# Kernel tuning notes

Hardware: AMD Instinct MI355X
Metric: run time of the kernel (lower is better)

Reference implementation:

```python
import jax, jax.numpy as jnp
import numpy as np

V, E, H, D1, D2, C = 32000, 500, 500, 800, 100, 2
B, T = 64, 400


def setup_inputs() -> dict:
    key = jax.random.key(0)
    ks = jax.random.split(key, 12)
    s = lambda fan_in, fan_out: float(np.sqrt(6.0 / (fan_in + fan_out)))  # xavier uniform
    u = lambda k, shape, lim: jax.random.uniform(k, shape, jnp.float32, -lim, lim)
    X = jax.random.randint(ks[0], (B, T), 0, V, dtype=jnp.int32)
    embed = u(ks[1], (V, E), s(V, E))
    # TF LSTMCell: kernel [input+hidden, 4*hidden], bias zeros, gate order i,j,f,o
    k1 = u(ks[2], (E + H, 4 * H), s(E + H, 4 * H))
    b1 = jnp.zeros((4 * H,), jnp.float32)
    k2 = u(ks[3], (H + H, 4 * H), s(H + H, 4 * H))
    b2 = jnp.zeros((4 * H,), jnp.float32)
    w1 = u(ks[4], (H, D1), s(H, D1)); bw1 = jnp.zeros((D1,), jnp.float32)
    w2 = u(ks[5], (D1, D2), s(D1, D2)); bw2 = jnp.zeros((D2,), jnp.float32)
    wp = u(ks[6], (D2, C), s(D2, C)); bp = jnp.zeros((C,), jnp.float32)
    return dict(X=X, embed=embed, k1=k1, b1=b1, k2=k2, b2=b2,
                w1=w1, bw1=bw1, w2=w2, bw2=bw2, wp=wp, bp=bp)


def _lstm(x_tbe, kernel, bias, hsize):
    """x_tbe: [T,B,in]; TF LSTMCell math with forget_bias=1.0. Returns all h: [T,B,H]."""
    Bn = x_tbe.shape[1]
    c0 = jnp.zeros((Bn, hsize), x_tbe.dtype)
    h0 = jnp.zeros((Bn, hsize), x_tbe.dtype)

    def step(carry, x_t):
        c, h = carry
        z = jnp.concatenate([x_t, h], axis=-1) @ kernel + bias
        i, j, f, o = jnp.split(z, 4, axis=-1)
        c = jax.nn.sigmoid(f + 1.0) * c + jax.nn.sigmoid(i) * jnp.tanh(j)
        h = jax.nn.sigmoid(o) * jnp.tanh(c)
        return (c, h), h

    _, hs = jax.lax.scan(step, (c0, h0), x_tbe)
    return hs


def reference(X, embed, k1, b1, k2, b2, w1, bw1, w2, bw2, wp, bp):
    # inference mode: dropout is identity
    x = embed[X]                      # [B,T,E]
    x = jnp.transpose(x, (1, 0, 2))   # [T,B,E]
    hs1 = _lstm(x, k1, b1, H)         # [T,B,H]
    hs2 = _lstm(hs1, k2, b2, H)       # [T,B,H]
    last = hs2[-1]                    # [B,H] last-step output of layer 2
    d1 = jax.nn.relu(last @ w1 + bw1)
    d2 = jax.nn.relu(d1 @ w2 + bw2)
    logits = d2 @ wp + bp             # [B,C]
    return logits
```

## Files before the change

### kernel.cpp

```cpp
#include <hip/hip_runtime.h>


#define NTHR 512
#define Tn 400
#define Hn 500

#define OFF_H1 0
#define OFF_H2 256000
#define OFF_C1 512000
#define OFF_C2 768000
#define OFF_D1 1024000
#define OFF_D2 1228800
#define WS_ZERO 1024000

__device__ __forceinline__ float qreduce(float v) {
    int t = __builtin_amdgcn_update_dpp(0, __float_as_int(v), 0xB1, 0xF, 0xF, true);
    v += __int_as_float(t);
    t = __builtin_amdgcn_update_dpp(0, __float_as_int(v), 0x4E, 0xF, 0xF, true);
    v += __int_as_float(t);
    return v;
}

__device__ __forceinline__ int wrow_map(int r) {
    int r2 = (r >= 512) ? r - 12 : r;
    if ((r >= 500 && r < 512) || r >= 1012) r2 = 0;
    return r2;
}

extern "C" __global__ void __launch_bounds__(NTHR)
rnn_step(const int* __restrict__ X, const float* __restrict__ embed,
         const float* __restrict__ k1, const float* __restrict__ b1g,
         const float* __restrict__ k2, const float* __restrict__ b2g,
         char* __restrict__ ws, int s)
{
    __shared__ float s_x[16384];
    __shared__ float s_w[2][8192];

    float* h1b = (float*)(ws + OFF_H1);
    float* h2b = (float*)(ws + OFF_H2);

    const int bid = blockIdx.x;
    const int tid = threadIdx.x;
    const int rr_ = bid >> 3;
    const int slice = (bid & 7) * 8 + (rr_ >> 2);
    const int btile = rr_ & 3;
    const int L = slice >> 5;
    const int ut = slice & 31;
    const int b0 = btile * 16;

    const bool active = L ? (s >= 1) : (s < Tn);
    if (!active) return;

    const int w = tid >> 6;
    const int l = tid & 63;
    const int ks = l & 3;
    const int cg = (l >> 2) & 7;
    const int bg = l >> 5;

    const float* Wm = L ? k2 : k1;
    const float* bv = L ? b2g : b1g;
    double* cb = (double*)(ws + (L ? OFF_C2 : OFF_C1));

    const int cur = s & 1, prv = cur ^ 1;
    const float* h1p = h1b + prv * 32000;
    const float* h2p = h2b + prv * 32000;
    float* houtT = (L ? h2b : h1b) + cur * 32000;
    const int t = L ? (s - 1) : s;
    const float* hlow = h1p;
    const float* hhigh = L ? h2p : h1p;

    const int wdr = l >> 4;
    const int wcq = l & 15;
    const int c_l = (4 * wcq) ^ (wdr << 3);
    const int wcol = (c_l >> 4) * 500 + min(ut * 16 + (c_l & 15), 496);

    const int xdr = l >> 2;
    const int xq4 = (l & 3) * 4;

    if (w == 7) {
        if (L == 0) {
            const int eb = l & 15, r = 496 + (l >> 4);
            const float v = embed[(size_t)X[(b0 + eb) * Tn + t] * 500 + r];
            s_x[r * 16 + eb] = v;
        } else {
            if (l < 16) {
                const int r = 496 + (l >> 2);
                const float4 v = *(const float4*)(hlow + r * 64 + b0 + (l & 3) * 4);
                *(float4*)&s_x[r * 16 + (l & 3) * 4] = v;
            }
        }
        if (l < 48) {
            const int r = 500 + (l >> 2);
            *(float4*)&s_x[r * 16 + (l & 3) * 4] = make_float4(0.f, 0.f, 0.f, 0.f);
        }
        if (l < 16) {
            const int r = 1008 + (l >> 2);
            const float4 v = *(const float4*)(hhigh + (r - 512) * 64 + b0 + (l & 3) * 4);
            *(float4*)&s_x[r * 16 + (l & 3) * 4] = v;
        }
        if (l < 48) {
            const int r = 1012 + (l >> 2);
            *(float4*)&s_x[r * 16 + (l & 3) * 4] = make_float4(0.f, 0.f, 0.f, 0.f);
        }
    }
    if (L == 0) {
        const int eb = l & 15, j = l >> 4;
        const int xid = X[(b0 + eb) * Tn + t];
        const float* er = embed + (size_t)xid * 500;
        #pragma unroll
        for (int c = 0; c < 4; ++c) {
            if (w < 7 || c < 3) {
                const int base = 128 * c + 16 * w;
                const float4 v = *(const float4*)(er + base + 4 * j);
                float* d = &s_x[(base + 4 * j) * 16 + eb];
                d[0] = v.x; d[16] = v.y; d[32] = v.z; d[48] = v.w;
            }
        }
        #pragma unroll
        for (int c = 4; c < 8; ++c) {
            if (!(w == 7 && c == 7)) {
                const int base = 128 * c + 16 * w;
                const float* src = hhigh + (base - 512 + xdr) * 64 + b0 + xq4;
                __builtin_amdgcn_global_load_lds(src, &s_x[base * 16], 16, 0, 0);
            }
        }
    } else {
        #pragma unroll
        for (int c = 0; c < 8; ++c) {
            if (!(w == 7 && (c == 3 || c == 7))) {
                const int base = 128 * c + 16 * w;
                const float* src = (c < 4)
                    ? (hlow + (base + xdr) * 64 + b0 + xq4)
                    : (hhigh + (base - 512 + xdr) * 64 + b0 + xq4);
                __builtin_amdgcn_global_load_lds(src, &s_x[base * 16], 16, 0, 0);
            }
        }
    }
    #pragma unroll
    for (int q = 0; q < 4; ++q) {
        const int lr = 16 * w + 4 * q;
        const int gr = wrow_map(lr + wdr);
        __builtin_amdgcn_global_load_lds(Wm + (size_t)gr * 2000 + wcol,
                                         &s_w[0][lr * 64], 16, 0, 0);
    }

    float4 acc[8][2];
    #pragma unroll
    for (int cc = 0; cc < 8; ++cc) {
        acc[cc][0] = make_float4(0.f, 0.f, 0.f, 0.f);
        acc[cc][1] = make_float4(0.f, 0.f, 0.f, 0.f);
    }

    #pragma unroll
    for (int c = 0; c < 8; ++c) {
        if (c < 7) {
            #pragma unroll
            for (int q = 0; q < 4; ++q) {
                const int lr = 16 * w + 4 * q;
                const int gr = wrow_map(128 * (c + 1) + lr + wdr);
                __builtin_amdgcn_global_load_lds(Wm + (size_t)gr * 2000 + wcol,
                                                 &s_w[(c + 1) & 1][lr * 64], 16, 0, 0);
            }
            asm volatile("s_waitcnt vmcnt(4)" ::: "memory");
        } else {
            asm volatile("s_waitcnt vmcnt(0)" ::: "memory");
        }
        __builtin_amdgcn_sched_barrier(0);
        const float* wb = s_w[c & 1];
        #pragma unroll
        for (int i = 0; i < 4; ++i) {
            const int lr = 16 * w + 4 * i + ks;
            const float4 wA = *(const float4*)&wb[lr * 64 + ((cg ^ ks) << 3)];
            const float4 wB = *(const float4*)&wb[lr * 64 + ((cg ^ ks) << 3) + 4];
            const float* xr = &s_x[(128 * c + lr) * 16 + bg * 8];
            const float4 xA = *(const float4*)(xr);
            const float4 xB = *(const float4*)(xr + 4);
#define ACCUM(CC, WS) \
    acc[CC][0].x = fmaf(WS, xA.x, acc[CC][0].x); \
    acc[CC][0].y = fmaf(WS, xA.y, acc[CC][0].y); \
    acc[CC][0].z = fmaf(WS, xA.z, acc[CC][0].z); \
    acc[CC][0].w = fmaf(WS, xA.w, acc[CC][0].w); \
    acc[CC][1].x = fmaf(WS, xB.x, acc[CC][1].x); \
    acc[CC][1].y = fmaf(WS, xB.y, acc[CC][1].y); \
    acc[CC][1].z = fmaf(WS, xB.z, acc[CC][1].z); \
    acc[CC][1].w = fmaf(WS, xB.w, acc[CC][1].w);
            ACCUM(0, wA.x) ACCUM(1, wA.y) ACCUM(2, wA.z) ACCUM(3, wA.w)
            ACCUM(4, wB.x) ACCUM(5, wB.y) ACCUM(6, wB.z) ACCUM(7, wB.w)
#undef ACCUM
        }
    }

    #pragma unroll
    for (int cc = 0; cc < 8; ++cc) {
        #pragma unroll
        for (int j = 0; j < 2; ++j) {
            acc[cc][j].x = qreduce(acc[cc][j].x);
            acc[cc][j].y = qreduce(acc[cc][j].y);
            acc[cc][j].z = qreduce(acc[cc][j].z);
            acc[cc][j].w = qreduce(acc[cc][j].w);
        }
    }
    if (ks == 0) {
        float* p0 = &s_w[0][w * 1024];
        #pragma unroll
        for (int cc = 0; cc < 8; ++cc) {
            const int col = cg * 8 + cc;
            #pragma unroll
            for (int j = 0; j < 2; ++j) {
                const int pos = (bg * 8 + 4 * j) ^ (4 * (cg & 3));
                *(float4*)&p0[col * 16 + pos] = acc[cc][j];
            }
        }
    }
    __syncthreads();

    if (tid < 256) {
        const int gb = tid & 15;
        const int uu = tid >> 4;
        const int u = ut * 16 + uu;
        if (u < Hn) {
            double z[4];
            #pragma unroll
            for (int g = 0; g < 4; ++g) {
                const int col = g * 16 + uu;
                const int pos = gb ^ (4 * ((col >> 3) & 3));
                double zz = 0.0;
                #pragma unroll
                for (int q = 0; q < 8; ++q)
                    zz += (double)s_w[0][q * 1024 + col * 16 + pos];
                z[g] = zz + (double)bv[g * 500 + u];
            }
            const double gi = 1.0 / (1.0 + exp(-z[0]));
            const double gf = 1.0 / (1.0 + exp(-(z[2] + 1.0)));
            const double go_ = 1.0 / (1.0 + exp(-z[3]));
            const int ci = u * 64 + b0 + gb;
            const double cnew = gf * cb[ci] + gi * tanh(z[1]);
            cb[ci] = cnew;
            houtT[ci] = (float)(go_ * tanh(cnew));
        }
    }
}

extern "C" __global__ void __launch_bounds__(256)
head1(const char* __restrict__ ws_c, const float* __restrict__ w1,
      const float* __restrict__ bw1, char* __restrict__ ws)
{
    const float* lastT = (const float*)(ws_c + OFF_H2);
    float* d1p = (float*)(ws + OFF_D1);
    const int o = blockIdx.x * 256 + threadIdx.x;
    if (o >= 51200) return;
    const int b = o / 800, j = o - b * 800;
    double acc = 0;
    for (int kk = 0; kk < 500; ++kk)
        acc += (double)lastT[kk * 64 + b] * (double)w1[(size_t)kk * 800 + j];
    acc += (double)bw1[j];
    d1p[b * 800 + j] = (float)fmax(acc, 0.0);
}

extern "C" __global__ void __launch_bounds__(256)
head2(const char* __restrict__ ws_c, const float* __restrict__ w2,
      const float* __restrict__ bw2, char* __restrict__ ws)
{
    const float* d1p = (const float*)(ws_c + OFF_D1);
    float* d2p = (float*)(ws + OFF_D2);
    const int o = blockIdx.x * 256 + threadIdx.x;
    if (o >= 6400) return;
    const int b = o / 100, j = o - b * 100;
    const float* dr = d1p + b * 800;
    double acc = 0;
    for (int kk = 0; kk < 800; ++kk)
        acc += (double)dr[kk] * (double)w2[(size_t)kk * 100 + j];
    acc += (double)bw2[j];
    d2p[b * 100 + j] = (float)fmax(acc, 0.0);
}

extern "C" __global__ void __launch_bounds__(128)
head3(const char* __restrict__ ws_c, const float* __restrict__ wpm,
      const float* __restrict__ bpv, float* __restrict__ out)
{
    const float* d2p = (const float*)(ws_c + OFF_D2);
    const int tid = threadIdx.x;
    const int b = tid >> 1, cc = tid & 1;
    const float* dr = d2p + b * 100;
    double acc = 0;
    for (int kk = 0; kk < 100; ++kk)
        acc += (double)dr[kk] * (double)wpm[kk * 2 + cc];
    acc += (double)bpv[cc];
    out[b * 2 + cc] = (float)acc;
}

extern "C" void kernel_launch(void* const* d_in, const int* in_sizes, int n_in,
                              void* d_out, int out_size, void* d_ws, size_t ws_size,
                              hipStream_t stream) {
    const int* X = (const int*)d_in[0];
    const float* embed = (const float*)d_in[1];
    const float* k1 = (const float*)d_in[2];
    const float* b1 = (const float*)d_in[3];
    const float* k2 = (const float*)d_in[4];
    const float* b2 = (const float*)d_in[5];
    const float* w1 = (const float*)d_in[6];
    const float* bw1 = (const float*)d_in[7];
    const float* w2 = (const float*)d_in[8];
    const float* bw2 = (const float*)d_in[9];
    const float* wpm = (const float*)d_in[10];
    const float* bpv = (const float*)d_in[11];
    char* ws = (char*)d_ws;

    hipMemsetAsync(d_ws, 0, WS_ZERO, stream);

    for (int s = 0; s <= Tn; ++s)
        rnn_step<<<256, NTHR, 0, stream>>>(X, embed, k1, b1, k2, b2, ws, s);

    head1<<<200, 256, 0, stream>>>(ws, w1, bw1, ws);
    head2<<<25, 256, 0, stream>>>(ws, w2, bw2, ws);
    head3<<<1, 128, 0, stream>>>(ws, wpm, bpv, (float*)d_out);
}
```

Before: 5.837 ms.

## Retile LSTM step microkernel to 8 gates x 16 batches per thread with swizzled LDS

Each thread now accumulates 8 gate columns across all 16 batch entries (acc 8x4 float4) and covers half as many k-rows, so every x load is reused across more weights. The x and weight tiles in LDS get XOR swizzles to cut bank conflicts. The final DPP reduction no longer writes only from ks==0 lanes: each lane selects one quarter of the reduced values, and partial sums go into two sets of slots that the gate stage then sums (16 partials). This raises register pressure per thread, which may lower occupancy.

```diff
diff --git a/kernel.cpp b/kernel.cpp
--- a/kernel.cpp
+++ b/kernel.cpp
@@ -13,12 +13,16 @@
 #define OFF_D2 1228800
 #define WS_ZERO 1024000
 
-__device__ __forceinline__ float qreduce(float v) {
+__device__ __forceinline__ float qreduce2(float v) {
     int t = __builtin_amdgcn_update_dpp(0, __float_as_int(v), 0xB1, 0xF, 0xF, true);
     v += __int_as_float(t);
     t = __builtin_amdgcn_update_dpp(0, __float_as_int(v), 0x4E, 0xF, 0xF, true);
     v += __int_as_float(t);
     return v;
+}
+
+__device__ __forceinline__ float4 sel4(int c, float4 a, float4 b) {
+    return make_float4(c ? a.x : b.x, c ? a.y : b.y, c ? a.z : b.z, c ? a.w : b.w);
 }
 
 __device__ __forceinline__ int wrow_map(int r) {
@@ -55,7 +59,7 @@
     const int l = tid & 63;
     const int ks = l & 3;
     const int cg = (l >> 2) & 7;
-    const int bg = l >> 5;
+    const int iL = l >> 5;
 
     const float* Wm = L ? k2 : k1;
     const float* bv = L ? b2g : b1g;
@@ -69,70 +73,85 @@
     const float* hlow = h1p;
     const float* hhigh = L ? h2p : h1p;
 
+    const int qlA = (l & 15) ^ (2 * (l >> 4));
+    const int qlB = qlA ^ 1;
+    const int wcolA = (qlA >> 2) * 500 + min(ut * 16 + 4 * (qlA & 3), 496);
+    const int wcolB = (qlB >> 2) * 500 + min(ut * 16 + 4 * (qlB & 3), 496);
     const int wdr = l >> 4;
-    const int wcq = l & 15;
-    const int c_l = (4 * wcq) ^ (wdr << 3);
-    const int wcol = (c_l >> 4) * 500 + min(ut * 16 + (c_l & 15), 496);
-
-    const int xdr = l >> 2;
-    const int xq4 = (l & 3) * 4;
-
-    if (w == 7) {
-        if (L == 0) {
-            const int eb = l & 15, r = 496 + (l >> 4);
-            const float v = embed[(size_t)X[(b0 + eb) * Tn + t] * 500 + r];
-            s_x[r * 16 + eb] = v;
-        } else {
+
+    const int xsw = 4 * ((l & 3) ^ ((l >> 2) & 3));
+
+    if (L == 0) {
+        const int eb = l & 15;
+        const int kq = l >> 4;
+        const float* er = embed + (size_t)X[(b0 + eb) * Tn + t] * 500;
+        const int bq = eb >> 2, bsw = eb & 3;
+        #pragma unroll
+        for (int c = 0; c < 4; ++c) {
+            if (w < 7 || c < 3) {
+                const int base = 128 * c + 16 * w + 4 * kq;
+                const float4 v = *(const float4*)(er + base);
+                s_x[(base + 0) * 16 + 4 * (bq ^ 0) + bsw] = v.x;
+                s_x[(base + 1) * 16 + 4 * (bq ^ 1) + bsw] = v.y;
+                s_x[(base + 2) * 16 + 4 * (bq ^ 2) + bsw] = v.z;
+                s_x[(base + 3) * 16 + 4 * (bq ^ 3) + bsw] = v.w;
+            }
+        }
+        #pragma unroll
+        for (int c = 4; c < 8; ++c) {
+            if (w < 7 || c < 7) {
+                const int base = 128 * c + 16 * w;
+                const float* src = hhigh + (base - 512 + (l >> 2)) * 64 + b0 + xsw;
+                __builtin_amdgcn_global_load_lds(src, &s_x[base * 16], 16, 0, 0);
+            }
+        }
+        if (w == 7) {
+            {
+                const int r = 496 + (l >> 4);
+                const int b = l & 15;
+                const float vv = embed[(size_t)X[(b0 + b) * Tn + t] * 500 + r];
+                s_x[r * 16 + 4 * ((b >> 2) ^ (r & 3)) + (b & 3)] = vv;
+            }
+            if (l < 16) {
+                const int r = 1008 + (l >> 2);
+                const float4 v = *(const float4*)(hhigh + (r - 512) * 64 + b0
+                                   + 4 * ((l & 3) ^ (r & 3)));
+                *(float4*)&s_x[r * 16 + 4 * (l & 3)] = v;
+            }
+            if (l < 48) {
+                const int r = 500 + (l >> 2);
+                *(float4*)&s_x[r * 16 + 4 * (l & 3)] = make_float4(0.f, 0.f, 0.f, 0.f);
+                const int r2 = 1012 + (l >> 2);
+                *(float4*)&s_x[r2 * 16 + 4 * (l & 3)] = make_float4(0.f, 0.f, 0.f, 0.f);
+            }
+        }
+    } else {
+        #pragma unroll
+        for (int c = 0; c < 8; ++c) {
+            if (w < 7 || (c != 3 && c != 7)) {
+                const int base = 128 * c + 16 * w;
+                const float* src = (c < 4)
+                    ? (hlow + (base + (l >> 2)) * 64 + b0 + xsw)
+                    : (hhigh + (base - 512 + (l >> 2)) * 64 + b0 + xsw);
+                __builtin_amdgcn_global_load_lds(src, &s_x[base * 16], 16, 0, 0);
+            }
+        }
+        if (w == 7) {
             if (l < 16) {
                 const int r = 496 + (l >> 2);
-                const float4 v = *(const float4*)(hlow + r * 64 + b0 + (l & 3) * 4);
-                *(float4*)&s_x[r * 16 + (l & 3) * 4] = v;
-            }
-        }
-        if (l < 48) {
-            const int r = 500 + (l >> 2);
-            *(float4*)&s_x[r * 16 + (l & 3) * 4] = make_float4(0.f, 0.f, 0.f, 0.f);
-        }
-        if (l < 16) {
-            const int r = 1008 + (l >> 2);
-            const float4 v = *(const float4*)(hhigh + (r - 512) * 64 + b0 + (l & 3) * 4);
-            *(float4*)&s_x[r * 16 + (l & 3) * 4] = v;
-        }
-        if (l < 48) {
-            const int r = 1012 + (l >> 2);
-            *(float4*)&s_x[r * 16 + (l & 3) * 4] = make_float4(0.f, 0.f, 0.f, 0.f);
-        }
-    }
-    if (L == 0) {
-        const int eb = l & 15, j = l >> 4;
-        const int xid = X[(b0 + eb) * Tn + t];
-        const float* er = embed + (size_t)xid * 500;
-        #pragma unroll
-        for (int c = 0; c < 4; ++c) {
-            if (w < 7 || c < 3) {
-                const int base = 128 * c + 16 * w;
-                const float4 v = *(const float4*)(er + base + 4 * j);
-                float* d = &s_x[(base + 4 * j) * 16 + eb];
-                d[0] = v.x; d[16] = v.y; d[32] = v.z; d[48] = v.w;
-            }
-        }
-        #pragma unroll
-        for (int c = 4; c < 8; ++c) {
-            if (!(w == 7 && c == 7)) {
-                const int base = 128 * c + 16 * w;
-                const float* src = hhigh + (base - 512 + xdr) * 64 + b0 + xq4;
-                __builtin_amdgcn_global_load_lds(src, &s_x[base * 16], 16, 0, 0);
-            }
-        }
-    } else {
-        #pragma unroll
-        for (int c = 0; c < 8; ++c) {
-            if (!(w == 7 && (c == 3 || c == 7))) {
-                const int base = 128 * c + 16 * w;
-                const float* src = (c < 4)
-                    ? (hlow + (base + xdr) * 64 + b0 + xq4)
-                    : (hhigh + (base - 512 + xdr) * 64 + b0 + xq4);
-                __builtin_amdgcn_global_load_lds(src, &s_x[base * 16], 16, 0, 0);
+                const float4 v = *(const float4*)(hlow + r * 64 + b0
+                                   + 4 * ((l & 3) ^ (r & 3)));
+                *(float4*)&s_x[r * 16 + 4 * (l & 3)] = v;
+                const int r2 = 1008 + (l >> 2);
+                const float4 v2 = *(const float4*)(hhigh + (r2 - 512) * 64 + b0
+                                    + 4 * ((l & 3) ^ (r2 & 3)));
+                *(float4*)&s_x[r2 * 16 + 4 * (l & 3)] = v2;
+            }
+            if (l < 48) {
+                const int r = 500 + (l >> 2);
+                *(float4*)&s_x[r * 16 + 4 * (l & 3)] = make_float4(0.f, 0.f, 0.f, 0.f);
+                const int r2 = 1012 + (l >> 2);
+                *(float4*)&s_x[r2 * 16 + 4 * (l & 3)] = make_float4(0.f, 0.f, 0.f, 0.f);
             }
         }
     }
@@ -140,16 +159,20 @@
     for (int q = 0; q < 4; ++q) {
         const int lr = 16 * w + 4 * q;
         const int gr = wrow_map(lr + wdr);
-        __builtin_amdgcn_global_load_lds(Wm + (size_t)gr * 2000 + wcol,
+        const int col = (q < 2) ? wcolA : wcolB;
+        __builtin_amdgcn_global_load_lds(Wm + (size_t)gr * 2000 + col,
                                          &s_w[0][lr * 64], 16, 0, 0);
     }
 
-    float4 acc[8][2];
+    float4 acc[8][4];
     #pragma unroll
     for (int cc = 0; cc < 8; ++cc) {
-        acc[cc][0] = make_float4(0.f, 0.f, 0.f, 0.f);
-        acc[cc][1] = make_float4(0.f, 0.f, 0.f, 0.f);
-    }
+        #pragma unroll
+        for (int j = 0; j < 4; ++j) acc[cc][j] = make_float4(0.f, 0.f, 0.f, 0.f);
+    }
+
+    const int woffA = (((cg ^ ks) << 1) ^ iL) << 2;
+    const int woffB = woffA ^ 4;
 
     #pragma unroll
     for (int c = 0; c < 8; ++c) {
@@ -158,7 +181,8 @@
             for (int q = 0; q < 4; ++q) {
                 const int lr = 16 * w + 4 * q;
                 const int gr = wrow_map(128 * (c + 1) + lr + wdr);
-                __builtin_amdgcn_global_load_lds(Wm + (size_t)gr * 2000 + wcol,
+                const int col = (q < 2) ? wcolA : wcolB;
+                __builtin_amdgcn_global_load_lds(Wm + (size_t)gr * 2000 + col,
                                                  &s_w[(c + 1) & 1][lr * 64], 16, 0, 0);
             }
             asm volatile("s_waitcnt vmcnt(4)" ::: "memory");
@@ -168,48 +192,54 @@
         __builtin_amdgcn_sched_barrier(0);
         const float* wb = s_w[c & 1];
         #pragma unroll
-        for (int i = 0; i < 4; ++i) {
-            const int lr = 16 * w + 4 * i + ks;
-            const float4 wA = *(const float4*)&wb[lr * 64 + ((cg ^ ks) << 3)];
-            const float4 wB = *(const float4*)&wb[lr * 64 + ((cg ^ ks) << 3) + 4];
-            const float* xr = &s_x[(128 * c + lr) * 16 + bg * 8];
-            const float4 xA = *(const float4*)(xr);
-            const float4 xB = *(const float4*)(xr + 4);
-#define ACCUM(CC, WS) \
-    acc[CC][0].x = fmaf(WS, xA.x, acc[CC][0].x); \
-    acc[CC][0].y = fmaf(WS, xA.y, acc[CC][0].y); \
-    acc[CC][0].z = fmaf(WS, xA.z, acc[CC][0].z); \
-    acc[CC][0].w = fmaf(WS, xA.w, acc[CC][0].w); \
-    acc[CC][1].x = fmaf(WS, xB.x, acc[CC][1].x); \
-    acc[CC][1].y = fmaf(WS, xB.y, acc[CC][1].y); \
-    acc[CC][1].z = fmaf(WS, xB.z, acc[CC][1].z); \
-    acc[CC][1].w = fmaf(WS, xB.w, acc[CC][1].w);
-            ACCUM(0, wA.x) ACCUM(1, wA.y) ACCUM(2, wA.z) ACCUM(3, wA.w)
-            ACCUM(4, wB.x) ACCUM(5, wB.y) ACCUM(6, wB.z) ACCUM(7, wB.w)
-#undef ACCUM
+        for (int i = 0; i < 2; ++i) {
+            const int rl = 8 * iL + 4 * i + ks;
+            const int lr = 16 * w + rl;
+            const float4 wA = *(const float4*)&wb[lr * 64 + woffA];
+            const float4 wB = *(const float4*)&wb[lr * 64 + woffB];
+            const float* xr = &s_x[(128 * c + lr) * 16];
+            const float4 x0 = *(const float4*)(xr + ((0 ^ ks) << 2));
+            const float4 x1 = *(const float4*)(xr + ((1 ^ ks) << 2));
+            const float4 x2 = *(const float4*)(xr + ((2 ^ ks) << 2));
+            const float4 x3 = *(const float4*)(xr + ((3 ^ ks) << 2));
+#define FMA4(CC, WS, XV, J) \
+    acc[CC][J].x = fmaf(WS, XV.x, acc[CC][J].x); \
+    acc[CC][J].y = fmaf(WS, XV.y, acc[CC][J].y); \
+    acc[CC][J].z = fmaf(WS, XV.z, acc[CC][J].z); \
+    acc[CC][J].w = fmaf(WS, XV.w, acc[CC][J].w);
+#define FMAC(CC, WS) FMA4(CC, WS, x0, 0) FMA4(CC, WS, x1, 1) \
+                     FMA4(CC, WS, x2, 2) FMA4(CC, WS, x3, 3)
+            FMAC(0, wA.x) FMAC(1, wA.y) FMAC(2, wA.z) FMAC(3, wA.w)
+            FMAC(4, wB.x) FMAC(5, wB.y) FMAC(6, wB.z) FMAC(7, wB.w)
+#undef FMAC
+#undef FMA4
         }
     }
 
     #pragma unroll
     for (int cc = 0; cc < 8; ++cc) {
         #pragma unroll
-        for (int j = 0; j < 2; ++j) {
-            acc[cc][j].x = qreduce(acc[cc][j].x);
-            acc[cc][j].y = qreduce(acc[cc][j].y);
-            acc[cc][j].z = qreduce(acc[cc][j].z);
-            acc[cc][j].w = qreduce(acc[cc][j].w);
-        }
-    }
-    if (ks == 0) {
-        float* p0 = &s_w[0][w * 1024];
-        #pragma unroll
-        for (int cc = 0; cc < 8; ++cc) {
-            const int col = cg * 8 + cc;
-            #pragma unroll
-            for (int j = 0; j < 2; ++j) {
-                const int pos = (bg * 8 + 4 * j) ^ (4 * (cg & 3));
-                *(float4*)&p0[col * 16 + pos] = acc[cc][j];
-            }
+        for (int j = 0; j < 4; ++j) {
+            acc[cc][j].x = qreduce2(acc[cc][j].x);
+            acc[cc][j].y = qreduce2(acc[cc][j].y);
+            acc[cc][j].z = qreduce2(acc[cc][j].z);
+            acc[cc][j].w = qreduce2(acc[cc][j].w);
+        }
+    }
+    {
+        float* P = &s_w[0][0];
+        const int set_off = iL * 8192 + w * 1024;
+        const int colA = 8 * cg + ks;
+        const int colB = colA + 4;
+        const int gsw = ((ks >> 1) ^ (cg & 3)) & 3;
+        #pragma unroll
+        for (int j = 0; j < 4; ++j) {
+            const float4 pa = sel4(ks & 2, sel4(ks & 1, acc[3][j], acc[2][j]),
+                                           sel4(ks & 1, acc[1][j], acc[0][j]));
+            const float4 pb = sel4(ks & 2, sel4(ks & 1, acc[7][j], acc[6][j]),
+                                           sel4(ks & 1, acc[5][j], acc[4][j]));
+            *(float4*)&P[set_off + colA * 16 + 4 * (j ^ gsw)] = pa;
+            *(float4*)&P[set_off + colB * 16 + 4 * (j ^ gsw)] = pb;
         }
     }
     __syncthreads();
@@ -219,15 +249,17 @@
         const int uu = tid >> 4;
         const int u = ut * 16 + uu;
         if (u < Hn) {
+            const float* P = &s_w[0][0];
             double z[4];
             #pragma unroll
             for (int g = 0; g < 4; ++g) {
                 const int col = g * 16 + uu;
-                const int pos = gb ^ (4 * ((col >> 3) & 3));
+                const int gsw = (((col >> 1) & 1) ^ ((col >> 3) & 3)) & 3;
+                const int pos = col * 16 + 4 * ((gb >> 2) ^ gsw) + (gb & 3);
                 double zz = 0.0;
                 #pragma unroll
-                for (int q = 0; q < 8; ++q)
-                    zz += (double)s_w[0][q * 1024 + col * 16 + pos];
+                for (int q = 0; q < 16; ++q)
+                    zz += (double)P[(q & 1) * 8192 + (q >> 1) * 1024 + pos];
                 z[g] = zz + (double)bv[g * 500 + u];
             }
             const double gi = 1.0 / (1.0 + exp(-z[0]));
```

Measured after the change: 13.73 ms. +135.2%, slower.
